# Kernel optimization log

Measured on AMD Instinct MI355X. Metric: run time of the kernel, lower is better.

## Reference

```python
import jax, jax.numpy as jnp
import numpy as np

DIM = 128
SUPPORT = 1
NL, NM, NG = 5, 20, 100
EPS_BN = 1e-5
EPS_NORM = 1e-12


def knn_idx(vertices, k):
    # vertices: (b, v, 3) -> (b, v, k) indices of k nearest (excluding self)
    sq = jnp.sum(vertices * vertices, axis=-1)  # (b, v)
    dist = -2.0 * jnp.einsum('bic,bjc->bij', vertices, vertices) + sq[:, :, None] + sq[:, None, :]
    _, idx = jax.lax.top_k(-dist, k + 1)  # smallest distances
    return idx[:, :, 1:]


def gather_nbr(t, idx):
    # t: (b, v, c), idx: (b, v, n) -> (b, v, n, c)
    b = t.shape[0]
    return t[jnp.arange(b)[:, None, None], idx]


def conv_layer(idx, vertices, fmap, W, bias, dirs):
    # idx: (b,v,n); fmap: (b,v,DIM); W: (DIM,(S+1)*DIM); bias: ((S+1)*DIM,); dirs: (3,S*DIM)
    nbrs = gather_nbr(vertices, idx)                      # (b,v,n,3)
    d = nbrs - vertices[:, :, None, :]
    d = d / jnp.maximum(jnp.linalg.norm(d, axis=-1, keepdims=True), EPS_NORM)
    sd = dirs / jnp.maximum(jnp.linalg.norm(dirs, axis=0, keepdims=True), EPS_NORM)
    theta = jax.nn.relu(jnp.einsum('bvnc,ck->bvnk', d, sd))  # (b,v,n,S*DIM)
    fo = fmap @ W + bias                                   # (b,v,(S+1)*DIM)
    center = fo[..., :DIM]
    supp = gather_nbr(fo[..., DIM:], idx)                  # (b,v,n,S*DIM)
    b_, v_, n_ = idx.shape
    act = (theta * supp).reshape(b_, v_, n_, SUPPORT, DIM)
    act = jnp.max(act, axis=2).sum(axis=2)                 # max over neighbors, sum over supports
    return center + act                                    # (b,v,DIM)


def bn_relu(x, gamma, beta):
    # training-mode BatchNorm1d over (batch, points) per channel, then ReLU
    mu = jnp.mean(x, axis=(0, 1))
    var = jnp.var(x, axis=(0, 1))
    return jax.nn.relu((x - mu) * jax.lax.rsqrt(var + EPS_BN) * gamma + beta)


def setup_inputs() -> dict:
    key = jax.random.key(0)
    ks = jax.random.split(key, 8)
    B, V = 2, 1024
    return {
        'vertices': jax.random.normal(ks[0], (B, V, 3), jnp.float32),
        'x': jax.random.normal(ks[1], (B, V, DIM), jnp.float32),
        'conv_W': jax.random.normal(ks[2], (6, DIM, (SUPPORT + 1) * DIM), jnp.float32) * 0.05,
        'conv_b': jax.random.normal(ks[3], (6, (SUPPORT + 1) * DIM), jnp.float32) * 0.05,
        'conv_dirs': jax.random.normal(ks[4], (6, 3, SUPPORT * DIM), jnp.float32),
        'bn_gamma': jnp.ones((6, DIM), jnp.float32),
        'bn_beta': jnp.zeros((6, DIM), jnp.float32),
        'down_W': jax.random.normal(ks[5], (3 * DIM, 2 * DIM), jnp.float32) * 0.05,
        'down_b': jax.random.normal(ks[6], (2 * DIM,), jnp.float32) * 0.05,
    }


def reference(vertices, x, conv_W, conv_b, conv_dirs, bn_gamma, bn_beta, down_W, down_b):
    il = knn_idx(vertices, NL)
    im = knn_idx(vertices, NM)
    ig = knn_idx(vertices, NG)
    # param index order: 0=l, 1=m0, 2=m1, 3=g0, 4=g1, 5=g2 (g2 unused, per source bug)
    fl = bn_relu(conv_layer(il, vertices, x, conv_W[0], conv_b[0], conv_dirs[0]), bn_gamma[0], bn_beta[0])
    fm = bn_relu(conv_layer(im, vertices, x, conv_W[1], conv_b[1], conv_dirs[1]), bn_gamma[1], bn_beta[1])
    fm = bn_relu(conv_layer(im, vertices, fm, conv_W[2], conv_b[2], conv_dirs[2]), bn_gamma[2], bn_beta[2])
    fg = bn_relu(conv_layer(ig, vertices, x, conv_W[3], conv_b[3], conv_dirs[3]), bn_gamma[3], bn_beta[3])
    fg = bn_relu(conv_layer(ig, vertices, fg, conv_W[4], conv_b[4], conv_dirs[4]), bn_gamma[4], bn_beta[4])
    # source reuses conv_g0 / bn_g0 for the third global layer
    fg = bn_relu(conv_layer(ig, vertices, fg, conv_W[3], conv_b[3], conv_dirs[3]), bn_gamma[3], bn_beta[3])
    out = jnp.concatenate([fl, fm, fg], axis=2)            # (b, v, 3*DIM)
    return jax.nn.relu(out @ down_W + down_b)              # (b, v, 2*DIM)
```

## Files before the change

kernel.cpp:

```cpp
#include <hip/hip_runtime.h>


__device__ __forceinline__ void do_gemm(
    const float* __restrict__ in, const float* __restrict__ stp,
    const float* __restrict__ gm, const float* __restrict__ bt,
    const float* __restrict__ W, const float* __restrict__ bi,
    float* __restrict__ out, int rb, char* smemc)
{
    float* rows  = (float*)smemc;
    float* wch   = rows + 1024;
    float* scale = wch + 4096;
    float* shift = scale + 128;
    int t = threadIdx.x;
    if (t < 128) {
        float sc = 1.0f, sf = 0.0f;
        if (stp) {
            float sm = 0.0f, sq = 0.0f;
            #pragma unroll 8
            for (int bk = 0; bk < 32; ++bk) {
                sm += stp[bk*256 + t];
                sq += stp[bk*256 + 128 + t];
            }
            float mu  = sm * (1.0f/2048.0f);
            float var = sq * (1.0f/2048.0f) - mu*mu;
            sc = rsqrtf(var + 1e-5f) * gm[t];
            sf = bt[t] - mu*sc;
        }
        scale[t] = sc; shift[t] = sf;
    }
    __syncthreads();
    int r0 = rb * 8;
    {
        float4 v = ((const float4*)(in + r0*128))[t];
        if (stp) {
            int c4 = (t & 31) << 2;
            v.x = fmaxf(v.x*scale[c4  ] + shift[c4  ], 0.0f);
            v.y = fmaxf(v.y*scale[c4+1] + shift[c4+1], 0.0f);
            v.z = fmaxf(v.z*scale[c4+2] + shift[c4+2], 0.0f);
            v.w = fmaxf(v.w*scale[c4+3] + shift[c4+3], 0.0f);
        }
        ((float4*)rows)[t] = v;
    }
    int cb = t & 63, rp = (t >> 6) << 1;
    const float* a0r = rows + rp*128;
    const float* a1r = a0r + 128;
    const float4* W4 = (const float4*)W;
    float4* wch4 = (float4*)wch;
    float4 acc0 = make_float4(0.f,0.f,0.f,0.f);
    float4 acc1 = make_float4(0.f,0.f,0.f,0.f);
    for (int c = 0; c < 8; ++c) {
        __syncthreads();
        #pragma unroll
        for (int i = 0; i < 4; ++i)
            wch4[t + 256*i] = W4[c*1024 + t + 256*i];
        __syncthreads();
        int kb = c*16;
        #pragma unroll
        for (int k = 0; k < 16; k += 4) {
            float4 a0 = *(const float4*)(a0r + kb + k);
            float4 a1 = *(const float4*)(a1r + kb + k);
            float4 w;
            w = wch4[(k+0)*64+cb];
            acc0.x += a0.x*w.x; acc0.y += a0.x*w.y; acc0.z += a0.x*w.z; acc0.w += a0.x*w.w;
            acc1.x += a1.x*w.x; acc1.y += a1.x*w.y; acc1.z += a1.x*w.z; acc1.w += a1.x*w.w;
            w = wch4[(k+1)*64+cb];
            acc0.x += a0.y*w.x; acc0.y += a0.y*w.y; acc0.z += a0.y*w.z; acc0.w += a0.y*w.w;
            acc1.x += a1.y*w.x; acc1.y += a1.y*w.y; acc1.z += a1.y*w.z; acc1.w += a1.y*w.w;
            w = wch4[(k+2)*64+cb];
            acc0.x += a0.z*w.x; acc0.y += a0.z*w.y; acc0.z += a0.z*w.z; acc0.w += a0.z*w.w;
            acc1.x += a1.z*w.x; acc1.y += a1.z*w.y; acc1.z += a1.z*w.z; acc1.w += a1.z*w.w;
            w = wch4[(k+3)*64+cb];
            acc0.x += a0.w*w.x; acc0.y += a0.w*w.y; acc0.z += a0.w*w.z; acc0.w += a0.w*w.w;
            acc1.x += a1.w*w.x; acc1.y += a1.w*w.y; acc1.z += a1.w*w.z; acc1.w += a1.w*w.w;
        }
    }
    float4 b4 = ((const float4*)bi)[cb];
    acc0.x += b4.x; acc0.y += b4.y; acc0.z += b4.z; acc0.w += b4.w;
    acc1.x += b4.x; acc1.y += b4.y; acc1.z += b4.z; acc1.w += b4.w;
    ((float4*)out)[(r0+rp  )*64 + cb] = acc0;
    ((float4*)out)[(r0+rp+1)*64 + cb] = acc1;
}

__global__ void k1_kernel(const float* __restrict__ verts, const float* __restrict__ dirs,
                          const float* __restrict__ x,
                          const float* __restrict__ convW, const float* __restrict__ convB,
                          int* __restrict__ idxout, float* __restrict__ sdn,
                          float* __restrict__ stp, float* __restrict__ fo)
{
    __shared__ __align__(16) char smem[21504];
    int t = threadIdx.x;
    int blk = blockIdx.x;

    if (blk >= 1280) {
        if (blk == 1472) {
            for (int i = t; i < 768; i += 256) {
                int l = i >> 7, k = i & 127;
                float a = dirs[l*384 + k];
                float b = dirs[l*384 + 128 + k];
                float c = dirs[l*384 + 256 + k];
                float nrm = sqrtf(a*a + b*b + c*c);
                float inv = 1.0f / fmaxf(nrm, 1e-12f);
                sdn[l*384 + k]       = a*inv;
                sdn[l*384 + 128 + k] = b*inv;
                sdn[l*384 + 256 + k] = c*inv;
            }
        } else {
            stp[(blk - 1280)*256 + t] = 0.0f;
        }
        return;
    }
    if (blk >= 512) {
        int g = blk - 512;
        int s = g >> 8, rb = g & 255;
        int wi = (s==0) ? 0 : (s==1) ? 1 : 3;
        do_gemm(x, (const float*)0, (const float*)0, (const float*)0,
                convW + wi*32768, convB + wi*256, fo + s*524288, rb, smem);
        return;
    }

    float* xs  = (float*)smem;
    float* ys  = xs + 1024;
    float* zs  = ys + 1024;
    float* sqs = zs + 1024;
    unsigned int* histBase = (unsigned int*)(smem + 16384);
    unsigned int* selBase  = (unsigned int*)(smem + 20480);

    int w = t >> 6, l = t & 63;
    int vglob = blk*4 + w;
    int b = vglob >> 10;
    int v = vglob & 1023;
    unsigned long long* keys = (unsigned long long*)smem + w*256;
    unsigned int* hist = histBase + w*256;
    unsigned int* sel  = selBase + w*4;

    const float* vb = verts + b * 3072;
    for (int i = t; i < 1024; i += 256) {
        float xx = vb[i*3+0], yy = vb[i*3+1], zz = vb[i*3+2];
        xs[i] = xx; ys[i] = yy; zs[i] = zz;
        sqs[i] = xx*xx + yy*yy + zz*zz;
    }
    __syncthreads();

    float cx = xs[v], cy = ys[v], cz = zs[v], csq = sqs[v];
    unsigned long long K16[16];
    #pragma unroll
    for (int q = 0; q < 16; ++q) {
        int j = q*64 + l;
        float dot = cx*xs[j] + cy*ys[j] + cz*zs[j];
        float d = -2.0f*dot + csq + sqs[j];
        unsigned int u = __float_as_uint(d);
        u = (u & 0x80000000u) ? ~u : (u | 0x80000000u);
        K16[q] = (((unsigned long long)u) << 32) | (unsigned long long)j;
    }
    #pragma unroll
    for (int i = 0; i < 4; ++i) hist[l*4 + i] = 0u;
    __syncthreads();

    #pragma unroll
    for (int q = 0; q < 16; ++q)
        atomicAdd(&hist[(unsigned int)(K16[q] >> 56)], 1u);
    __syncthreads();

    {
        unsigned int h0 = hist[l*4], h1 = hist[l*4+1], h2 = hist[l*4+2], h3 = hist[l*4+3];
        unsigned int c1 = h0, c2 = h0+h1, c3 = h0+h1+h2, T = c3+h3;
        unsigned int xacc = T;
        #pragma unroll
        for (int off = 1; off < 64; off <<= 1) {
            unsigned int y = __shfl_up(xacc, off, 64);
            if (l >= off) xacc += y;
        }
        unsigned int P = xacc - T;
        unsigned int ex[4] = {P, P+c1, P+c2, P+c3};
        unsigned int hh[4] = {h0, h1, h2, h3};
        #pragma unroll
        for (int i = 0; i < 4; ++i) {
            if (ex[i] < 101u && ex[i] + hh[i] >= 101u) {
                sel[0] = (unsigned int)(l*4 + i);
                sel[1] = 101u - ex[i];
            }
        }
    }
    __syncthreads();
    unsigned int P8 = sel[0], rank2 = sel[1];
    #pragma unroll
    for (int i = 0; i < 4; ++i) hist[l*4 + i] = 0u;
    __syncthreads();

    #pragma unroll
    for (int q = 0; q < 16; ++q)
        if ((unsigned int)(K16[q] >> 56) == P8)
            atomicAdd(&hist[(unsigned int)(K16[q] >> 48) & 0xFFu], 1u);
    __syncthreads();

    {
        unsigned int h0 = hist[l*4], h1 = hist[l*4+1], h2 = hist[l*4+2], h3 = hist[l*4+3];
        unsigned int c1 = h0, c2 = h0+h1, c3 = h0+h1+h2, T = c3+h3;
        unsigned int xacc = T;
        #pragma unroll
        for (int off = 1; off < 64; off <<= 1) {
            unsigned int y = __shfl_up(xacc, off, 64);
            if (l >= off) xacc += y;
        }
        unsigned int P = xacc - T;
        unsigned int ex[4] = {P, P+c1, P+c2, P+c3};
        unsigned int hh[4] = {h0, h1, h2, h3};
        #pragma unroll
        for (int i = 0; i < 4; ++i) {
            if (ex[i] < rank2 && ex[i] + hh[i] >= rank2) {
                sel[2] = (P8 << 8) | (unsigned int)(l*4 + i);
                sel[3] = 0u;
            }
        }
    }
    __syncthreads();
    unsigned int P16 = sel[2];

    #pragma unroll
    for (int q = 0; q < 16; ++q) {
        if ((unsigned int)(K16[q] >> 48) <= P16) {
            unsigned int pos = atomicAdd(&sel[3], 1u);
            if (pos < 256u) keys[pos] = K16[q];
        }
    }
    __syncthreads();
    unsigned int cnt = sel[3];

    unsigned long long K[4];
    #pragma unroll
    for (int q = 0; q < 4; ++q) {
        unsigned int e = (unsigned int)(l*4 + q);
        K[q] = (e < cnt) ? keys[e] : 0xFFFFFFFFFFFFFFFFULL;
    }

    auto cswap = [&](int qa, int qb, int k) {
        int e = (l << 2) + qa;
        bool up = ((e & k) == 0);
        unsigned long long a = K[qa], bb2 = K[qb];
        unsigned long long mn = a < bb2 ? a : bb2;
        unsigned long long mx = a < bb2 ? bb2 : a;
        K[qa] = up ? mn : mx;
        K[qb] = up ? mx : mn;
    };
    #pragma unroll
    for (int k = 2; k <= 256; k <<= 1) {
        for (int j = k >> 1; j >= 4; j >>= 1) {
            int lj = j >> 2;
            #pragma unroll
            for (int q = 0; q < 4; ++q) {
                unsigned long long other = __shfl_xor(K[q], lj, 64);
                int e = (l << 2) + q;
                bool up = ((e & k) == 0);
                bool lower = ((l & lj) == 0);
                bool takeMin = (lower == up);
                unsigned long long mn = K[q] < other ? K[q] : other;
                unsigned long long mx = K[q] < other ? other : K[q];
                K[q] = takeMin ? mn : mx;
            }
        }
        if (k >= 4) { cswap(0, 2, k); cswap(1, 3, k); }
        cswap(0, 1, k); cswap(2, 3, k);
    }

    #pragma unroll
    for (int q = 0; q < 4; ++q) {
        int e = l*4 + q;
        if (e >= 1 && e <= 100)
            idxout[vglob*100 + (e-1)] = (int)(K[q] & 0xFFFFFFFFu);
    }
}

__global__ void agg_kernel(const int* __restrict__ idx, const float* __restrict__ verts,
                           const float* __restrict__ sdn, const float* __restrict__ fo,
                           int n0, int n1, int n2, int d0, int d1, int d2,
                           float* o0, float* o1, float* o2,
                           float* s0p, float* s1p, float* s2p)
{
    __shared__ float4 ds4s[200];
    __shared__ int jss[200];
    int slot = blockIdx.y;
    int n  = slot==0 ? n0 : slot==1 ? n1 : n2;
    int dI = slot==0 ? d0 : slot==1 ? d1 : d2;
    float* outp = slot==0 ? o0 : slot==1 ? o1 : o2;
    float* stp  = slot==0 ? s0p : slot==1 ? s1p : s2p;
    const float* fos = fo + slot * 524288;
    const float* sd = sdn + dI * 384;

    int t = threadIdx.x;
    int h = t >> 7, tt = t & 127;
    float4* ds4 = ds4s + h*100;
    int* js = jss + h*100;
    int r = blockIdx.x*2 + h;
    int b = r >> 10;

    if (tt < n) {
        int j = idx[r*100 + tt];
        js[tt] = j;
        const float* pj = verts + (b*1024 + j)*3;
        const float* pv = verts + r*3;
        float dx = pj[0]-pv[0], dy = pj[1]-pv[1], dz = pj[2]-pv[2];
        float nm = sqrtf(dx*dx + dy*dy + dz*dz);
        float inv = 1.0f / fmaxf(nm, 1e-12f);
        ds4[tt] = make_float4(dx*inv, dy*inv, dz*inv, 0.0f);
    }
    __syncthreads();
    float s0 = sd[tt], s1 = sd[128+tt], s2 = sd[256+tt];
    int bb = b * 1024;
    float m = -3.0e38f;
    for (int q = 0; q < n; q += 5) {
        float th[5];
        const float* p[5];
        #pragma unroll
        for (int u = 0; u < 5; ++u) {
            float4 dq = ds4[q+u];
            th[u] = fmaxf(dq.x*s0 + dq.y*s1 + dq.z*s2, 0.0f);
            p[u] = fos + (size_t)(bb + js[q+u])*256 + 128 + tt;
        }
        float vv[5];
        #pragma unroll
        for (int u = 0; u < 5; ++u) vv[u] = *p[u];
        #pragma unroll
        for (int u = 0; u < 5; ++u) m = fmaxf(m, th[u]*vv[u]);
    }
    float val = fos[r*256 + tt] + m;
    outp[r*128 + tt] = val;
    float* bank = stp + (r & 31)*256;
    atomicAdd(&bank[tt], val);
    atomicAdd(&bank[128+tt], val*val);
}

__global__ void gemm2_kernel(
    const float* inA, const float* stA, const float* gA, const float* beA,
    const float* WA, const float* biA, float* foA,
    const float* inB, const float* stB, const float* gB, const float* beB,
    const float* WB, const float* biB, float* foB)
{
    __shared__ __align__(16) char smem[21504];
    if (blockIdx.y == 0)
        do_gemm(inA, stA, gA, beA, WA, biA, foA, blockIdx.x, smem);
    else
        do_gemm(inB, stB, gB, beB, WB, biB, foB, blockIdx.x, smem);
}

__global__ void down_kernel(
    const float* __restrict__ p0, const float* __restrict__ s0p,
    const float* __restrict__ g0, const float* __restrict__ be0,
    const float* __restrict__ p1, const float* __restrict__ s1p,
    const float* __restrict__ g1, const float* __restrict__ be1,
    const float* __restrict__ p2, const float* __restrict__ s2p,
    const float* __restrict__ g2, const float* __restrict__ be2,
    const float* __restrict__ dW, const float* __restrict__ db,
    float* __restrict__ out)
{
    __shared__ float rows[8*384];
    __shared__ float wch[16*256];
    __shared__ float scale[384], shift[384];
    int t = threadIdx.x;
    int r0 = blockIdx.x * 8;
    for (int c = t; c < 384; c += 256) {
        int seg = c >> 7, cc = c & 127;
        const float* stp = seg==0 ? s0p : seg==1 ? s1p : s2p;
        const float* g   = seg==0 ? g0  : seg==1 ? g1  : g2;
        const float* be  = seg==0 ? be0 : seg==1 ? be1 : be2;
        float sm = 0.0f, sq = 0.0f;
        #pragma unroll 8
        for (int bk = 0; bk < 32; ++bk) {
            sm += stp[bk*256 + cc];
            sq += stp[bk*256 + 128 + cc];
        }
        float mu  = sm * (1.0f/2048.0f);
        float var = sq * (1.0f/2048.0f) - mu*mu;
        float s = rsqrtf(var + 1e-5f) * g[cc];
        scale[c] = s;
        shift[c] = be[cc] - mu*s;
    }
    __syncthreads();
    for (int q = t; q < 768; q += 256) {
        int row = q / 96, rem = q - row*96;
        int c4 = rem << 2;
        int seg = c4 >> 7, cc = c4 & 127;
        const float* ps = seg==0 ? p0 : seg==1 ? p1 : p2;
        float4 v = *(const float4*)(ps + (r0+row)*128 + cc);
        v.x = fmaxf(v.x*scale[c4  ] + shift[c4  ], 0.0f);
        v.y = fmaxf(v.y*scale[c4+1] + shift[c4+1], 0.0f);
        v.z = fmaxf(v.z*scale[c4+2] + shift[c4+2], 0.0f);
        v.w = fmaxf(v.w*scale[c4+3] + shift[c4+3], 0.0f);
        *(float4*)&rows[row*384 + c4] = v;
    }
    int cb = t & 63, rp = (t >> 6) << 1;
    const float* a0r = rows + rp*384;
    const float* a1r = a0r + 384;
    const float4* W4 = (const float4*)dW;
    float4* wch4 = (float4*)wch;
    float4 acc0 = make_float4(0.f,0.f,0.f,0.f);
    float4 acc1 = make_float4(0.f,0.f,0.f,0.f);
    for (int c = 0; c < 24; ++c) {
        __syncthreads();
        #pragma unroll
        for (int i = 0; i < 4; ++i)
            wch4[t + 256*i] = W4[c*1024 + t + 256*i];
        __syncthreads();
        int kb = c*16;
        #pragma unroll
        for (int k = 0; k < 16; k += 4) {
            float4 a0 = *(const float4*)(a0r + kb + k);
            float4 a1 = *(const float4*)(a1r + kb + k);
            float4 w;
            w = wch4[(k+0)*64+cb];
            acc0.x += a0.x*w.x; acc0.y += a0.x*w.y; acc0.z += a0.x*w.z; acc0.w += a0.x*w.w;
            acc1.x += a1.x*w.x; acc1.y += a1.x*w.y; acc1.z += a1.x*w.z; acc1.w += a1.x*w.w;
            w = wch4[(k+1)*64+cb];
            acc0.x += a0.y*w.x; acc0.y += a0.y*w.y; acc0.z += a0.y*w.z; acc0.w += a0.y*w.w;
            acc1.x += a1.y*w.x; acc1.y += a1.y*w.y; acc1.z += a1.y*w.z; acc1.w += a1.y*w.w;
            w = wch4[(k+2)*64+cb];
            acc0.x += a0.z*w.x; acc0.y += a0.z*w.y; acc0.z += a0.z*w.z; acc0.w += a0.z*w.w;
            acc1.x += a1.z*w.x; acc1.y += a1.z*w.y; acc1.z += a1.z*w.z; acc1.w += a1.z*w.w;
            w = wch4[(k+3)*64+cb];
            acc0.x += a0.w*w.x; acc0.y += a0.w*w.y; acc0.z += a0.w*w.z; acc0.w += a0.w*w.w;
            acc1.x += a1.w*w.x; acc1.y += a1.w*w.y; acc1.z += a1.w*w.z; acc1.w += a1.w*w.w;
        }
    }
    float4 b4 = ((const float4*)db)[cb];
    float4 o0, o1;
    o0.x = fmaxf(acc0.x + b4.x, 0.0f); o0.y = fmaxf(acc0.y + b4.y, 0.0f);
    o0.z = fmaxf(acc0.z + b4.z, 0.0f); o0.w = fmaxf(acc0.w + b4.w, 0.0f);
    o1.x = fmaxf(acc1.x + b4.x, 0.0f); o1.y = fmaxf(acc1.y + b4.y, 0.0f);
    o1.z = fmaxf(acc1.z + b4.z, 0.0f); o1.w = fmaxf(acc1.w + b4.w, 0.0f);
    ((float4*)out)[(r0+rp  )*64 + cb] = o0;
    ((float4*)out)[(r0+rp+1)*64 + cb] = o1;
}

extern "C" void kernel_launch(void* const* d_in, const int* in_sizes, int n_in,
                              void* d_out, int out_size, void* d_ws, size_t ws_size,
                              hipStream_t stream)
{
    (void)in_sizes; (void)n_in; (void)out_size; (void)ws_size;
    const float* verts = (const float*)d_in[0];
    const float* x     = (const float*)d_in[1];
    const float* convW = (const float*)d_in[2];
    const float* convB = (const float*)d_in[3];
    const float* dirs  = (const float*)d_in[4];
    const float* gam   = (const float*)d_in[5];
    const float* bet   = (const float*)d_in[6];
    const float* dW    = (const float*)d_in[7];
    const float* db    = (const float*)d_in[8];
    float* out = (float*)d_out;

    char* ws = (char*)d_ws;
    int*   idxb = (int*)(ws);
    float* sdn  = (float*)(ws + 819200);
    float* stp  = (float*)(ws + 828416);
    float* fo   = (float*)(ws + 1025024);
    float* p0   = (float*)(ws + 7316480);
    float* p1   = (float*)(ws + 8365056);
    float* p2   = (float*)(ws + 9413632);
    float* p3   = (float*)(ws + 10462208);
    float* p4   = (float*)(ws + 11510784);
    float* p5   = (float*)(ws + 12559360);

    const float* nf = (const float*)0;
    float* nw = (float*)0;
    float* stL0 = stp,         *stL1 = stp + 8192, *stL2 = stp + 16384;
    float* stL3 = stp + 24576, *stL4 = stp + 32768, *stL5 = stp + 40960;

    k1_kernel<<<1473, 256, 0, stream>>>(verts, dirs, x, convW, convB,
                                        idxb, sdn, stp, fo);
    agg_kernel<<<dim3(1024,3), 256, 0, stream>>>(
        idxb, verts, sdn, fo, 5, 20, 100, 0, 1, 3,
        p0, p1, p3, stL0, stL1, stL3);
    gemm2_kernel<<<dim3(256,2), 256, 0, stream>>>(
        p1, stL1, gam + 128, bet + 128, convW + 65536,  convB + 512,  fo,
        p3, stL3, gam + 384, bet + 384, convW + 131072, convB + 1024, fo + 524288);
    agg_kernel<<<dim3(1024,2), 256, 0, stream>>>(
        idxb, verts, sdn, fo, 20, 100, 0, 2, 4, 0,
        p2, p4, nw, stL2, stL4, nw);
    gemm2_kernel<<<dim3(256,1), 256, 0, stream>>>(
        p4, stL4, gam + 512, bet + 512, convW + 98304, convB + 768, fo,
        nf, nf, nf, nf, nf, nf, nw);
    agg_kernel<<<dim3(1024,1), 256, 0, stream>>>(
        idxb, verts, sdn, fo, 100, 0, 0, 3, 0, 0,
        p5, nw, nw, stL5, nw, nw);
    down_kernel<<<256, 256, 0, stream>>>(
        p0, stL0, gam, bet,
        p2, stL2, gam + 256, bet + 256,
        p5, stL5, gam + 384, bet + 384,
        dW, db, out);
}
```

Baseline: 187.8 us.

## Split neighbor max across two half-blocks per vertex in aggregation kernel

```diff
diff --git a/kernel.cpp b/kernel.cpp
--- a/kernel.cpp
+++ b/kernel.cpp
@@ -276,8 +276,9 @@
                            float* o0, float* o1, float* o2,
                            float* s0p, float* s1p, float* s2p)
 {
-    __shared__ float4 ds4s[200];
-    __shared__ int jss[200];
+    __shared__ float4 ds4[100];
+    __shared__ int js[100];
+    __shared__ float pm[2][128];
     int slot = blockIdx.y;
     int n  = slot==0 ? n0 : slot==1 ? n1 : n2;
     int dI = slot==0 ? d0 : slot==1 ? d1 : d2;
@@ -288,45 +289,53 @@
 
     int t = threadIdx.x;
     int h = t >> 7, tt = t & 127;
-    float4* ds4 = ds4s + h*100;
-    int* js = jss + h*100;
-    int r = blockIdx.x*2 + h;
+    int r = blockIdx.x;
     int b = r >> 10;
 
-    if (tt < n) {
-        int j = idx[r*100 + tt];
-        js[tt] = j;
+    if (t < n) {
+        int j = idx[r*100 + t];
+        js[t] = j;
         const float* pj = verts + (b*1024 + j)*3;
         const float* pv = verts + r*3;
         float dx = pj[0]-pv[0], dy = pj[1]-pv[1], dz = pj[2]-pv[2];
         float nm = sqrtf(dx*dx + dy*dy + dz*dz);
         float inv = 1.0f / fmaxf(nm, 1e-12f);
-        ds4[tt] = make_float4(dx*inv, dy*inv, dz*inv, 0.0f);
+        ds4[t] = make_float4(dx*inv, dy*inv, dz*inv, 0.0f);
     }
     __syncthreads();
     float s0 = sd[tt], s1 = sd[128+tt], s2 = sd[256+tt];
     int bb = b * 1024;
+    int nh = (n + 1) >> 1;
+    int qs = h * nh;
+    int qe = min(n, qs + nh);
     float m = -3.0e38f;
-    for (int q = 0; q < n; q += 5) {
-        float th[5];
-        const float* p[5];
-        #pragma unroll
-        for (int u = 0; u < 5; ++u) {
-            float4 dq = ds4[q+u];
+    for (int q0 = qs; q0 < qe; q0 += 10) {
+        float th[10], vv[10];
+        #pragma unroll
+        for (int u = 0; u < 10; ++u) {
+            int q = q0 + u;
+            int qc = (q < qe) ? q : qs;
+            float4 dq = ds4[qc];
             th[u] = fmaxf(dq.x*s0 + dq.y*s1 + dq.z*s2, 0.0f);
-            p[u] = fos + (size_t)(bb + js[q+u])*256 + 128 + tt;
-        }
-        float vv[5];
-        #pragma unroll
-        for (int u = 0; u < 5; ++u) vv[u] = *p[u];
-        #pragma unroll
-        for (int u = 0; u < 5; ++u) m = fmaxf(m, th[u]*vv[u]);
-    }
-    float val = fos[r*256 + tt] + m;
-    outp[r*128 + tt] = val;
-    float* bank = stp + (r & 31)*256;
-    atomicAdd(&bank[tt], val);
-    atomicAdd(&bank[128+tt], val*val);
+            vv[u] = fos[(size_t)(bb + js[qc])*256 + 128 + tt];
+        }
+        #pragma unroll
+        for (int u = 0; u < 10; ++u) {
+            int q = q0 + u;
+            float prod = th[u]*vv[u];
+            m = fmaxf(m, (q < qe) ? prod : -3.0e38f);
+        }
+    }
+    pm[h][tt] = m;
+    __syncthreads();
+    if (h == 0) {
+        float mm = fmaxf(pm[0][tt], pm[1][tt]);
+        float val = fos[r*256 + tt] + mm;
+        outp[r*128 + tt] = val;
+        float* bank = stp + (r & 31)*256;
+        atomicAdd(&bank[tt], val);
+        atomicAdd(&bank[128+tt], val*val);
+    }
 }
 
 __global__ void gemm2_kernel(
@@ -465,19 +474,19 @@
 
     k1_kernel<<<1473, 256, 0, stream>>>(verts, dirs, x, convW, convB,
                                         idxb, sdn, stp, fo);
-    agg_kernel<<<dim3(1024,3), 256, 0, stream>>>(
+    agg_kernel<<<dim3(2048,3), 256, 0, stream>>>(
         idxb, verts, sdn, fo, 5, 20, 100, 0, 1, 3,
         p0, p1, p3, stL0, stL1, stL3);
     gemm2_kernel<<<dim3(256,2), 256, 0, stream>>>(
         p1, stL1, gam + 128, bet + 128, convW + 65536,  convB + 512,  fo,
         p3, stL3, gam + 384, bet + 384, convW + 131072, convB + 1024, fo + 524288);
-    agg_kernel<<<dim3(1024,2), 256, 0, stream>>>(
+    agg_kernel<<<dim3(2048,2), 256, 0, stream>>>(
         idxb, verts, sdn, fo, 20, 100, 0, 2, 4, 0,
         p2, p4, nw, stL2, stL4, nw);
     gemm2_kernel<<<dim3(256,1), 256, 0, stream>>>(
         p4, stL4, gam + 512, bet + 512, convW + 98304, convB + 768, fo,
         nf, nf, nf, nf, nf, nf, nw);
-    agg_kernel<<<dim3(1024,1), 256, 0, stream>>>(
+    agg_kernel<<<dim3(2048,1), 256, 0, stream>>>(
         idxb, verts, sdn, fo, 100, 0, 0, 3, 0, 0,
         p5, nw, nw, stL5, nw, nw);
     down_kernel<<<256, 256, 0, stream>>>(
```

After: 190.6 us. Within noise of the previous version (+1.5%).
